# Performance work log

Hardware: AMD Instinct MI355X
Metric: run time of the kernel (lower is better)

Reference implementation:

```python
import jax, jax.numpy as jnp
import numpy as np

B, T, D, H, W = 512, 4096, 8, 16, 16  # batch, timesteps, data_size, hidden_size, width_size


def lipswish(x):
    return 0.909 * jax.nn.silu(x)


def _linear_params(key, out_f, in_f):
    kw, kb = jax.random.split(key)
    lim = 1.0 / np.sqrt(in_f)
    w = jax.random.uniform(kw, (out_f, in_f), minval=-lim, maxval=lim, dtype=jnp.float32)
    b = jax.random.uniform(kb, (out_f,), minval=-lim, maxval=lim, dtype=jnp.float32)
    return w, b


def setup_inputs() -> dict:
    key = jax.random.key(0)
    ks = jax.random.split(key, 9)
    ts = jnp.arange(T, dtype=jnp.float32)
    ys = jax.random.normal(ks[0], (B, T, D), dtype=jnp.float32)
    # initial MLP: (D+1) -> W -> H, relu hidden, identity final
    iW1, ib1 = _linear_params(ks[1], W, D + 1)
    iW2, ib2 = _linear_params(ks[2], H, W)
    # vf MLP: (H+1) -> W -> H, lipswish hidden, tanh final; scale=False -> ones (identity)
    vW1, vb1 = _linear_params(ks[3], W, H + 1)
    vW2, vb2 = _linear_params(ks[4], H, W)
    # cvf MLP: (H+1) -> W -> H*D, lipswish hidden, tanh final; scale=False -> ones
    cW1, cb1 = _linear_params(ks[5], W, H + 1)
    cW2, cb2 = _linear_params(ks[6], H * D, W)
    # readout: H -> 1
    rW, rb = _linear_params(ks[7], 1, H)
    return dict(ts=ts, ys=ys, iW1=iW1, ib1=ib1, iW2=iW2, ib2=ib2,
                vW1=vW1, vb1=vb1, vW2=vW2, vb2=vb2,
                cW1=cW1, cb1=cb1, cW2=cW2, cb2=cb2, rW=rW, rb=rb)


def reference(ts, ys, iW1, ib1, iW2, ib2, vW1, vb1, vW2, vb2,
              cW1, cb1, cW2, cb2, rW, rb):
    Bn, Tn, Dn = ys.shape
    Hn = iW2.shape[0]
    # initial hidden state: initial MLP on concat([t0, y0])
    init_in = jnp.concatenate([jnp.broadcast_to(ts[0], (Bn, 1)), ys[:, 0]], axis=1)  # (B, D+1)
    y0 = jax.nn.relu(init_in @ iW1.T + ib1) @ iW2.T + ib2  # (B, H)
    # Euler with dt=1 on integer-spaced ts: control increment = ys[n+1]-ys[n]
    dX = jnp.swapaxes(ys[:, 1:] - ys[:, :-1], 0, 1)  # (T-1, B, D)
    t_steps = ts[0] + jnp.arange(Tn - 1, dtype=ys.dtype)  # (T-1,)

    def step(y, inp):
        t, dx = inp  # scalar, (B, D)
        z = jnp.concatenate([jnp.broadcast_to(t, (Bn, 1)), y], axis=1)  # (B, H+1)
        f = jnp.tanh(lipswish(z @ vW1.T + vb1) @ vW2.T + vb2)           # (B, H) drift
        g = jnp.tanh(lipswish(z @ cW1.T + cb1) @ cW2.T + cb2)           # (B, H*D)
        g = g.reshape(Bn, Hn, Dn)
        y = y + f + jnp.einsum('bhd,bd->bh', g, dx)  # dt = 1.0
        return y, None

    yT, _ = jax.lax.scan(step, y0, (t_steps, dX))
    saved = jnp.stack([y0, yT], axis=1)  # SaveAt(t0=True, t1=True) -> (B, 2, H)
    return saved @ rW.T + rb  # (B, 2, 1)
```

## Files before the change

### kernel.cpp

```cpp
#include <hip/hip_runtime.h>

#define T_LEN 4096

typedef float v2f __attribute__((ext_vector_type(2)));
typedef float v4f __attribute__((ext_vector_type(4)));

__device__ __forceinline__ float frcp(float x) { return __builtin_amdgcn_rcpf(x); }
__device__ __forceinline__ float fexp2(float x) { return __builtin_amdgcn_exp2f(x); }

__device__ __forceinline__ void pk_fma_v(v2f& acc, v2f w, v2f s) {
  asm("v_pk_fma_f32 %0, %1, %2, %0" : "+v"(acc) : "v"(w), "v"(s));
}

template <int CTRL>
__device__ __forceinline__ float dpp_add(float x) {
  int t = __builtin_amdgcn_mov_dpp(__float_as_int(x), CTRL, 0xF, 0xF, true);
  return x + __int_as_float(t);
}

__device__ __forceinline__ void cfence() { asm volatile("" ::: "memory"); }

#define NLN2f (-0.6931471805599453f)

__device__ __forceinline__ float readout_lds(const float* cb,
                                             const float* __restrict__ rW,
                                             float rb0) {
  v4f a = *(const v4f*)(cb + 64);
  v4f b = *(const v4f*)(cb + 68);
  v4f c = *(const v4f*)(cb + 72);
  v4f d = *(const v4f*)(cb + 76);
  float o = rb0;
  o = fmaf(rW[0],  a.x, o); o = fmaf(rW[1],  a.y, o);
  o = fmaf(rW[2],  a.z, o); o = fmaf(rW[3],  a.w, o);
  o = fmaf(rW[4],  b.x, o); o = fmaf(rW[5],  b.y, o);
  o = fmaf(rW[6],  b.z, o); o = fmaf(rW[7],  b.w, o);
  o = fmaf(rW[8],  c.x, o); o = fmaf(rW[9],  c.y, o);
  o = fmaf(rW[10], c.z, o); o = fmaf(rW[11], c.w, o);
  o = fmaf(rW[12], d.x, o); o = fmaf(rW[13], d.y, o);
  o = fmaf(rW[14], d.z, o); o = fmaf(rW[15], d.w, o);
  return o;
}

__global__ __launch_bounds__(64) void disc_kernel(
    const float* __restrict__ ts, const float* __restrict__ ys,
    const float* __restrict__ iW1, const float* __restrict__ ib1,
    const float* __restrict__ iW2, const float* __restrict__ ib2,
    const float* __restrict__ vW1, const float* __restrict__ vb1,
    const float* __restrict__ vW2, const float* __restrict__ vb2,
    const float* __restrict__ cW1, const float* __restrict__ cb1,
    const float* __restrict__ cW2, const float* __restrict__ cb2,
    const float* __restrict__ rW, const float* __restrict__ rb,
    float* __restrict__ out)
{
  const int b   = blockIdx.x;
  const int l   = threadIdx.x;
  const int h16 = l & 15;
  const int p   = (l >> 4) & 1;
  const int hf  = l >> 2;
  const int d0  = (2 * l) & 7;
  const int q4  = 4 * (l & 3);
  const int ywslot = ((l & 3) == 0) ? (64 + hf) : (80 + l);

  __shared__ __align__(16) float sbuf[16];
  __shared__ __align__(16) float cbuf[160];
  __shared__ __align__(16) float xbuf[1024];

  const float* __restrict__ ysb = ys + (size_t)b * (T_LEN * 8);

  const float NL2E = -1.4426950408889634f;
  const float TSW  = 2.0f * 1.4426950408889634f * 0.909f;
  const float TSB  = 2.0f * 1.4426950408889634f;

  float w1t, b1m;
  v2f W1y2[8];
  {
    const float* W1 = p ? cW1 : vW1;
    const float* bv = p ? cb1 : vb1;
    w1t = NL2E * W1[h16 * 17];
    b1m = NL2E * bv[h16];
#pragma unroll
    for (int k = 0; k < 8; ++k) {
      v2f w; w.x = NL2E * W1[h16 * 17 + 1 + 2 * k];
             w.y = NL2E * W1[h16 * 17 + 2 + 2 * k];
      W1y2[k] = w;
    }
  }
  v2f W2q[2];
#pragma unroll
  for (int j = 0; j < 2; ++j) {
    v2f w; w.x = TSW * vW2[hf * 16 + q4 + 2 * j];
           w.y = TSW * vW2[hf * 16 + q4 + 2 * j + 1];
    W2q[j] = w;
  }
  v2f G0p[8], G1p[8];
#pragma unroll
  for (int k = 0; k < 8; ++k) {
    v2f c0; c0.x = TSW * cW2[(2 * l) * 16 + 2 * k]; c0.y = TSW * cW2[(2 * l) * 16 + 2 * k + 1];
    G0p[k] = c0;
    v2f c1; c1.x = TSW * cW2[(2 * l + 1) * 16 + 2 * k]; c1.y = TSW * cW2[(2 * l + 1) * 16 + 2 * k + 1];
    G1p[k] = c1;
  }
  const float b2p  = TSB * vb2[hf];
  const float bg0p = TSB * cb2[2 * l];
  const float bg1p = TSB * cb2[2 * l + 1];

  const float t0 = ts[0];

  float y_own;
  {
    float acc = ib1[h16] + iW1[h16 * 9] * t0;
#pragma unroll
    for (int d = 0; d < 8; ++d) acc = fmaf(iW1[h16 * 9 + 1 + d], ysb[d], acc);
    sbuf[h16] = fmaxf(acc, 0.0f);
    cfence();
    float acc2 = ib2[h16];
#pragma unroll
    for (int k = 0; k < 16; ++k) acc2 = fmaf(iW2[h16 * 16 + k], sbuf[k], acc2);
    cbuf[64 + h16] = acc2;
    cfence();
    y_own = cbuf[64 + hf];
  }

  {
    const float o = readout_lds(cbuf, rW, rb[0]);
    if (l == 0) out[2 * b] = o;
  }

  const int CLAMP = T_LEN * 8 - 4;
  float4 A, Bq, Cq, Dq;
  {
    const int f0 = l * 8;
    A  = *(const float4*)(ysb + min(f0,      CLAMP));
    Bq = *(const float4*)(ysb + min(f0 + 4,  CLAMP));
    Cq = *(const float4*)(ysb + min(f0 + 8,  CLAMP));
    Dq = *(const float4*)(ysb + min(f0 + 12, CLAMP));
    float4 e0, e1;
    e0.x = Cq.x - A.x;  e0.y = Cq.y - A.y;  e0.z = Cq.z - A.z;  e0.w = Cq.w - A.w;
    e1.x = Dq.x - Bq.x; e1.y = Dq.y - Bq.y; e1.z = Dq.z - Bq.z; e1.w = Dq.w - Bq.w;
    *(float4*)(xbuf + l * 8)     = e0;
    *(float4*)(xbuf + l * 8 + 4) = e1;
    cfence();
  }

  float t = t0;
  for (int c = 0; c < 64; ++c) {
    {
      const int cn = min(c + 1, 63);
      const int f0 = cn * 512 + l * 8;
      A  = *(const float4*)(ysb + min(f0,      CLAMP));
      Bq = *(const float4*)(ysb + min(f0 + 4,  CLAMP));
      Cq = *(const float4*)(ysb + min(f0 + 8,  CLAMP));
      Dq = *(const float4*)(ysb + min(f0 + 12, CLAMP));
    }
    const float* __restrict__ xb = xbuf + (c & 1) * 512;
    const int base = c * 64;
    const int nsteps = min(64, (T_LEN - 1) - base);
    for (int j = 0; j < nsteps; ++j) {
      const v4f ya = *(const v4f*)(cbuf + 64);
      const v4f yb = *(const v4f*)(cbuf + 68);
      const v4f yc = *(const v4f*)(cbuf + 72);
      const v4f yd = *(const v4f*)(cbuf + 76);
      const v2f dx = *(const v2f*)(xb + j * 8 + d0);

      const float m_t = fmaf(w1t, t, b1m);
      v2f ma; ma.x = m_t;  ma.y = 0.0f;
      v2f mb; mb.x = 0.0f; mb.y = 0.0f;
      pk_fma_v(ma, W1y2[0], ya.xy);
      pk_fma_v(ma, W1y2[1], ya.zw);
      pk_fma_v(ma, W1y2[2], yb.xy);
      pk_fma_v(ma, W1y2[3], yb.zw);
      pk_fma_v(mb, W1y2[4], yc.xy);
      pk_fma_v(mb, W1y2[5], yc.zw);
      pk_fma_v(mb, W1y2[6], yd.xy);
      pk_fma_v(mb, W1y2[7], yd.zw);
      const v2f ms = ma + mb;
      const float m = ms.x + ms.y;

      const float eM = fexp2(m);
      const float s  = (m * NLN2f) * frcp(1.0f + eM);

      cbuf[l] = s;
      cfence();
      const v4f g0 = *(const v4f*)(cbuf + 16);
      const v4f g1 = *(const v4f*)(cbuf + 20);
      const v4f g2 = *(const v4f*)(cbuf + 24);
      const v4f g3 = *(const v4f*)(cbuf + 28);
      const v4f sf = *(const v4f*)(cbuf + q4);

      v2f ga; ga.x = bg0p; ga.y = 0.0f;
      v2f gc; gc.x = 0.0f; gc.y = 0.0f;
      v2f gb; gb.x = bg1p; gb.y = 0.0f;
      v2f gd; gd.x = 0.0f; gd.y = 0.0f;
      pk_fma_v(ga, G0p[0], g0.xy); pk_fma_v(ga, G0p[1], g0.zw);
      pk_fma_v(ga, G0p[2], g1.xy); pk_fma_v(ga, G0p[3], g1.zw);
      pk_fma_v(gc, G0p[4], g2.xy); pk_fma_v(gc, G0p[5], g2.zw);
      pk_fma_v(gc, G0p[6], g3.xy); pk_fma_v(gc, G0p[7], g3.zw);
      pk_fma_v(gb, G1p[0], g0.xy); pk_fma_v(gb, G1p[1], g0.zw);
      pk_fma_v(gb, G1p[2], g1.xy); pk_fma_v(gb, G1p[3], g1.zw);
      pk_fma_v(gd, G1p[4], g2.xy); pk_fma_v(gd, G1p[5], g2.zw);
      pk_fma_v(gd, G1p[6], g3.xy); pk_fma_v(gd, G1p[7], g3.zw);

      v2f fa; fa.x = 0.0f; fa.y = 0.0f;
      pk_fma_v(fa, W2q[0], sf.xy);
      pk_fma_v(fa, W2q[1], sf.zw);
      float fp = fa.x + fa.y;
      fp = dpp_add<0xB1>(fp);
      fp = dpp_add<0x4E>(fp);
      const float farg = fp + b2p;

      const v2f gs0 = ga + gc;
      const v2f gs1 = gb + gd;
      const float g0v = fmaf(-2.0f, frcp(1.0f + fexp2(gs0.x + gs0.y)), 1.0f);
      const float g1v = fmaf(-2.0f, frcp(1.0f + fexp2(gs1.x + gs1.y)), 1.0f);
      const float fv  = fmaf(-2.0f, frcp(1.0f + fexp2(farg)), 1.0f);

      float pr = fmaf(g0v, dx.x, g1v * dx.y);
      pr = dpp_add<0xB1>(pr);
      pr = dpp_add<0x4E>(pr);

      y_own = y_own + (fv + pr);
      cbuf[ywslot] = y_own;
      cfence();
      t += 1.0f;
    }
    float* xbn = xbuf + ((c + 1) & 1) * 512;
    float4 e0, e1;
    e0.x = Cq.x - A.x;  e0.y = Cq.y - A.y;  e0.z = Cq.z - A.z;  e0.w = Cq.w - A.w;
    e1.x = Dq.x - Bq.x; e1.y = Dq.y - Bq.y; e1.z = Dq.z - Bq.z; e1.w = Dq.w - Bq.w;
    *(float4*)(xbn + l * 8)     = e0;
    *(float4*)(xbn + l * 8 + 4) = e1;
    cfence();
  }

  {
    const float o = readout_lds(cbuf, rW, rb[0]);
    if (l == 0) out[2 * b + 1] = o;
  }
}

extern "C" void kernel_launch(void* const* d_in, const int* in_sizes, int n_in,
                              void* d_out, int out_size, void* d_ws, size_t ws_size,
                              hipStream_t stream) {
  (void)in_sizes; (void)n_in; (void)out_size; (void)d_ws; (void)ws_size;
  const float* ts  = (const float*)d_in[0];
  const float* ys  = (const float*)d_in[1];
  const float* iW1 = (const float*)d_in[2];
  const float* ib1 = (const float*)d_in[3];
  const float* iW2 = (const float*)d_in[4];
  const float* ib2 = (const float*)d_in[5];
  const float* vW1 = (const float*)d_in[6];
  const float* vb1 = (const float*)d_in[7];
  const float* vW2 = (const float*)d_in[8];
  const float* vb2 = (const float*)d_in[9];
  const float* cW1 = (const float*)d_in[10];
  const float* cb1 = (const float*)d_in[11];
  const float* cW2 = (const float*)d_in[12];
  const float* cb2 = (const float*)d_in[13];
  const float* rW  = (const float*)d_in[14];
  const float* rb  = (const float*)d_in[15];
  float* out = (float*)d_out;
  hipLaunchKernelGGL(disc_kernel, dim3(512), dim3(64), 0, stream,
                     ts, ys, iW1, ib1, iW2, ib2, vW1, vb1, vW2, vb2,
                     cW1, cb1, cW2, cb2, rW, rb, out);
}
```

Before: 1.195 ms.

## Process two batch items per wavefront with interleaved independent recurrences

Each 64-lane block now advances two batch elements at once, with separate LDS state and control-increment buffers, and the instruction streams of the two recurrences are interleaved. The grid is halved to 256 blocks. The aim is to hide the latency of the serial per-step chain (LDS round trips, DPP reductions, exp/rcp) by giving the scheduler independent work within one wave. The cost is twice the instructions issued per wave and half as many waves, which on a device with many SIMDs may leave more of them idle.

```diff
diff --git a/kernel.cpp b/kernel.cpp
--- a/kernel.cpp
+++ b/kernel.cpp
@@ -52,7 +52,7 @@
     const float* __restrict__ rW, const float* __restrict__ rb,
     float* __restrict__ out)
 {
-  const int b   = blockIdx.x;
+  const int b0  = blockIdx.x * 2;
   const int l   = threadIdx.x;
   const int h16 = l & 15;
   const int p   = (l >> 4) & 1;
@@ -61,11 +61,15 @@
   const int q4  = 4 * (l & 3);
   const int ywslot = ((l & 3) == 0) ? (64 + hf) : (80 + l);
 
-  __shared__ __align__(16) float sbuf[16];
-  __shared__ __align__(16) float cbuf[160];
-  __shared__ __align__(16) float xbuf[1024];
-
-  const float* __restrict__ ysb = ys + (size_t)b * (T_LEN * 8);
+  __shared__ __align__(16) float sbuf0[16];
+  __shared__ __align__(16) float sbuf1[16];
+  __shared__ __align__(16) float cbuf0[160];
+  __shared__ __align__(16) float cbuf1[160];
+  __shared__ __align__(16) float xbuf0[1024];
+  __shared__ __align__(16) float xbuf1[1024];
+
+  const float* __restrict__ ysb0 = ys + (size_t)b0 * (T_LEN * 8);
+  const float* __restrict__ ysb1 = ysb0 + (size_t)(T_LEN * 8);
 
   const float NL2E = -1.4426950408889634f;
   const float TSW  = 2.0f * 1.4426950408889634f * 0.909f;
@@ -106,39 +110,65 @@
 
   const float t0 = ts[0];
 
-  float y_own;
-  {
-    float acc = ib1[h16] + iW1[h16 * 9] * t0;
-#pragma unroll
-    for (int d = 0; d < 8; ++d) acc = fmaf(iW1[h16 * 9 + 1 + d], ysb[d], acc);
-    sbuf[h16] = fmaxf(acc, 0.0f);
+  float y_own0, y_own1;
+  {
+    float a0 = ib1[h16] + iW1[h16 * 9] * t0;
+    float a1 = a0;
+#pragma unroll
+    for (int d = 0; d < 8; ++d) {
+      const float w = iW1[h16 * 9 + 1 + d];
+      a0 = fmaf(w, ysb0[d], a0);
+      a1 = fmaf(w, ysb1[d], a1);
+    }
+    sbuf0[h16] = fmaxf(a0, 0.0f);
+    sbuf1[h16] = fmaxf(a1, 0.0f);
     cfence();
-    float acc2 = ib2[h16];
-#pragma unroll
-    for (int k = 0; k < 16; ++k) acc2 = fmaf(iW2[h16 * 16 + k], sbuf[k], acc2);
-    cbuf[64 + h16] = acc2;
+    float c0 = ib2[h16];
+    float c1 = ib2[h16];
+#pragma unroll
+    for (int k = 0; k < 16; ++k) {
+      const float w = iW2[h16 * 16 + k];
+      c0 = fmaf(w, sbuf0[k], c0);
+      c1 = fmaf(w, sbuf1[k], c1);
+    }
+    cbuf0[64 + h16] = c0;
+    cbuf1[64 + h16] = c1;
     cfence();
-    y_own = cbuf[64 + hf];
-  }
-
-  {
-    const float o = readout_lds(cbuf, rW, rb[0]);
-    if (l == 0) out[2 * b] = o;
+    y_own0 = cbuf0[64 + hf];
+    y_own1 = cbuf1[64 + hf];
+  }
+
+  {
+    const float rb0 = rb[0];
+    const float o0 = readout_lds(cbuf0, rW, rb0);
+    const float o1 = readout_lds(cbuf1, rW, rb0);
+    if (l == 0) {
+      out[2 * b0]     = o0;
+      out[2 * b0 + 2] = o1;
+    }
   }
 
   const int CLAMP = T_LEN * 8 - 4;
-  float4 A, Bq, Cq, Dq;
+  float4 A0, B0, C0, D0, A1, B1, C1, D1;
   {
     const int f0 = l * 8;
-    A  = *(const float4*)(ysb + min(f0,      CLAMP));
-    Bq = *(const float4*)(ysb + min(f0 + 4,  CLAMP));
-    Cq = *(const float4*)(ysb + min(f0 + 8,  CLAMP));
-    Dq = *(const float4*)(ysb + min(f0 + 12, CLAMP));
+    A0 = *(const float4*)(ysb0 + min(f0,      CLAMP));
+    B0 = *(const float4*)(ysb0 + min(f0 + 4,  CLAMP));
+    C0 = *(const float4*)(ysb0 + min(f0 + 8,  CLAMP));
+    D0 = *(const float4*)(ysb0 + min(f0 + 12, CLAMP));
+    A1 = *(const float4*)(ysb1 + min(f0,      CLAMP));
+    B1 = *(const float4*)(ysb1 + min(f0 + 4,  CLAMP));
+    C1 = *(const float4*)(ysb1 + min(f0 + 8,  CLAMP));
+    D1 = *(const float4*)(ysb1 + min(f0 + 12, CLAMP));
     float4 e0, e1;
-    e0.x = Cq.x - A.x;  e0.y = Cq.y - A.y;  e0.z = Cq.z - A.z;  e0.w = Cq.w - A.w;
-    e1.x = Dq.x - Bq.x; e1.y = Dq.y - Bq.y; e1.z = Dq.z - Bq.z; e1.w = Dq.w - Bq.w;
-    *(float4*)(xbuf + l * 8)     = e0;
-    *(float4*)(xbuf + l * 8 + 4) = e1;
+    e0.x = C0.x - A0.x; e0.y = C0.y - A0.y; e0.z = C0.z - A0.z; e0.w = C0.w - A0.w;
+    e1.x = D0.x - B0.x; e1.y = D0.y - B0.y; e1.z = D0.z - B0.z; e1.w = D0.w - B0.w;
+    *(float4*)(xbuf0 + l * 8)     = e0;
+    *(float4*)(xbuf0 + l * 8 + 4) = e1;
+    e0.x = C1.x - A1.x; e0.y = C1.y - A1.y; e0.z = C1.z - A1.z; e0.w = C1.w - A1.w;
+    e1.x = D1.x - B1.x; e1.y = D1.y - B1.y; e1.z = D1.z - B1.z; e1.w = D1.w - B1.w;
+    *(float4*)(xbuf1 + l * 8)     = e0;
+    *(float4*)(xbuf1 + l * 8 + 4) = e1;
     cfence();
   }
 
@@ -147,94 +177,149 @@
     {
       const int cn = min(c + 1, 63);
       const int f0 = cn * 512 + l * 8;
-      A  = *(const float4*)(ysb + min(f0,      CLAMP));
-      Bq = *(const float4*)(ysb + min(f0 + 4,  CLAMP));
-      Cq = *(const float4*)(ysb + min(f0 + 8,  CLAMP));
-      Dq = *(const float4*)(ysb + min(f0 + 12, CLAMP));
-    }
-    const float* __restrict__ xb = xbuf + (c & 1) * 512;
+      A0 = *(const float4*)(ysb0 + min(f0,      CLAMP));
+      B0 = *(const float4*)(ysb0 + min(f0 + 4,  CLAMP));
+      C0 = *(const float4*)(ysb0 + min(f0 + 8,  CLAMP));
+      D0 = *(const float4*)(ysb0 + min(f0 + 12, CLAMP));
+      A1 = *(const float4*)(ysb1 + min(f0,      CLAMP));
+      B1 = *(const float4*)(ysb1 + min(f0 + 4,  CLAMP));
+      C1 = *(const float4*)(ysb1 + min(f0 + 8,  CLAMP));
+      D1 = *(const float4*)(ysb1 + min(f0 + 12, CLAMP));
+    }
+    const float* __restrict__ xb0 = xbuf0 + (c & 1) * 512;
+    const float* __restrict__ xb1 = xbuf1 + (c & 1) * 512;
     const int base = c * 64;
     const int nsteps = min(64, (T_LEN - 1) - base);
     for (int j = 0; j < nsteps; ++j) {
-      const v4f ya = *(const v4f*)(cbuf + 64);
-      const v4f yb = *(const v4f*)(cbuf + 68);
-      const v4f yc = *(const v4f*)(cbuf + 72);
-      const v4f yd = *(const v4f*)(cbuf + 76);
-      const v2f dx = *(const v2f*)(xb + j * 8 + d0);
+      const v4f ya0 = *(const v4f*)(cbuf0 + 64);
+      const v4f yb0 = *(const v4f*)(cbuf0 + 68);
+      const v4f yc0 = *(const v4f*)(cbuf0 + 72);
+      const v4f yd0 = *(const v4f*)(cbuf0 + 76);
+      const v4f ya1 = *(const v4f*)(cbuf1 + 64);
+      const v4f yb1 = *(const v4f*)(cbuf1 + 68);
+      const v4f yc1 = *(const v4f*)(cbuf1 + 72);
+      const v4f yd1 = *(const v4f*)(cbuf1 + 76);
+      const v2f dx0 = *(const v2f*)(xb0 + j * 8 + d0);
+      const v2f dx1 = *(const v2f*)(xb1 + j * 8 + d0);
 
       const float m_t = fmaf(w1t, t, b1m);
-      v2f ma; ma.x = m_t;  ma.y = 0.0f;
-      v2f mb; mb.x = 0.0f; mb.y = 0.0f;
-      pk_fma_v(ma, W1y2[0], ya.xy);
-      pk_fma_v(ma, W1y2[1], ya.zw);
-      pk_fma_v(ma, W1y2[2], yb.xy);
-      pk_fma_v(ma, W1y2[3], yb.zw);
-      pk_fma_v(mb, W1y2[4], yc.xy);
-      pk_fma_v(mb, W1y2[5], yc.zw);
-      pk_fma_v(mb, W1y2[6], yd.xy);
-      pk_fma_v(mb, W1y2[7], yd.zw);
-      const v2f ms = ma + mb;
-      const float m = ms.x + ms.y;
-
-      const float eM = fexp2(m);
-      const float s  = (m * NLN2f) * frcp(1.0f + eM);
-
-      cbuf[l] = s;
+      v2f ma0; ma0.x = m_t;  ma0.y = 0.0f;
+      v2f mb0; mb0.x = 0.0f; mb0.y = 0.0f;
+      v2f ma1; ma1.x = m_t;  ma1.y = 0.0f;
+      v2f mb1; mb1.x = 0.0f; mb1.y = 0.0f;
+      pk_fma_v(ma0, W1y2[0], ya0.xy); pk_fma_v(ma1, W1y2[0], ya1.xy);
+      pk_fma_v(ma0, W1y2[1], ya0.zw); pk_fma_v(ma1, W1y2[1], ya1.zw);
+      pk_fma_v(ma0, W1y2[2], yb0.xy); pk_fma_v(ma1, W1y2[2], yb1.xy);
+      pk_fma_v(ma0, W1y2[3], yb0.zw); pk_fma_v(ma1, W1y2[3], yb1.zw);
+      pk_fma_v(mb0, W1y2[4], yc0.xy); pk_fma_v(mb1, W1y2[4], yc1.xy);
+      pk_fma_v(mb0, W1y2[5], yc0.zw); pk_fma_v(mb1, W1y2[5], yc1.zw);
+      pk_fma_v(mb0, W1y2[6], yd0.xy); pk_fma_v(mb1, W1y2[6], yd1.xy);
+      pk_fma_v(mb0, W1y2[7], yd0.zw); pk_fma_v(mb1, W1y2[7], yd1.zw);
+      const v2f ms0 = ma0 + mb0;
+      const v2f ms1 = ma1 + mb1;
+      const float m0 = ms0.x + ms0.y;
+      const float m1 = ms1.x + ms1.y;
+
+      const float eM0 = fexp2(m0);
+      const float eM1 = fexp2(m1);
+      const float s0 = (m0 * NLN2f) * frcp(1.0f + eM0);
+      const float s1 = (m1 * NLN2f) * frcp(1.0f + eM1);
+
+      cbuf0[l] = s0;
+      cbuf1[l] = s1;
       cfence();
-      const v4f g0 = *(const v4f*)(cbuf + 16);
-      const v4f g1 = *(const v4f*)(cbuf + 20);
-      const v4f g2 = *(const v4f*)(cbuf + 24);
-      const v4f g3 = *(const v4f*)(cbuf + 28);
-      const v4f sf = *(const v4f*)(cbuf + q4);
-
-      v2f ga; ga.x = bg0p; ga.y = 0.0f;
-      v2f gc; gc.x = 0.0f; gc.y = 0.0f;
-      v2f gb; gb.x = bg1p; gb.y = 0.0f;
-      v2f gd; gd.x = 0.0f; gd.y = 0.0f;
-      pk_fma_v(ga, G0p[0], g0.xy); pk_fma_v(ga, G0p[1], g0.zw);
-      pk_fma_v(ga, G0p[2], g1.xy); pk_fma_v(ga, G0p[3], g1.zw);
-      pk_fma_v(gc, G0p[4], g2.xy); pk_fma_v(gc, G0p[5], g2.zw);
-      pk_fma_v(gc, G0p[6], g3.xy); pk_fma_v(gc, G0p[7], g3.zw);
-      pk_fma_v(gb, G1p[0], g0.xy); pk_fma_v(gb, G1p[1], g0.zw);
-      pk_fma_v(gb, G1p[2], g1.xy); pk_fma_v(gb, G1p[3], g1.zw);
-      pk_fma_v(gd, G1p[4], g2.xy); pk_fma_v(gd, G1p[5], g2.zw);
-      pk_fma_v(gd, G1p[6], g3.xy); pk_fma_v(gd, G1p[7], g3.zw);
-
-      v2f fa; fa.x = 0.0f; fa.y = 0.0f;
-      pk_fma_v(fa, W2q[0], sf.xy);
-      pk_fma_v(fa, W2q[1], sf.zw);
-      float fp = fa.x + fa.y;
-      fp = dpp_add<0xB1>(fp);
-      fp = dpp_add<0x4E>(fp);
-      const float farg = fp + b2p;
-
-      const v2f gs0 = ga + gc;
-      const v2f gs1 = gb + gd;
-      const float g0v = fmaf(-2.0f, frcp(1.0f + fexp2(gs0.x + gs0.y)), 1.0f);
-      const float g1v = fmaf(-2.0f, frcp(1.0f + fexp2(gs1.x + gs1.y)), 1.0f);
-      const float fv  = fmaf(-2.0f, frcp(1.0f + fexp2(farg)), 1.0f);
-
-      float pr = fmaf(g0v, dx.x, g1v * dx.y);
-      pr = dpp_add<0xB1>(pr);
-      pr = dpp_add<0x4E>(pr);
-
-      y_own = y_own + (fv + pr);
-      cbuf[ywslot] = y_own;
+      const v4f g00 = *(const v4f*)(cbuf0 + 16);
+      const v4f g10 = *(const v4f*)(cbuf0 + 20);
+      const v4f g20 = *(const v4f*)(cbuf0 + 24);
+      const v4f g30 = *(const v4f*)(cbuf0 + 28);
+      const v4f sf0 = *(const v4f*)(cbuf0 + q4);
+      const v4f g01 = *(const v4f*)(cbuf1 + 16);
+      const v4f g11 = *(const v4f*)(cbuf1 + 20);
+      const v4f g21 = *(const v4f*)(cbuf1 + 24);
+      const v4f g31 = *(const v4f*)(cbuf1 + 28);
+      const v4f sf1 = *(const v4f*)(cbuf1 + q4);
+
+      v2f ga0; ga0.x = bg0p; ga0.y = 0.0f;
+      v2f gc0; gc0.x = 0.0f; gc0.y = 0.0f;
+      v2f gb0; gb0.x = bg1p; gb0.y = 0.0f;
+      v2f gd0; gd0.x = 0.0f; gd0.y = 0.0f;
+      v2f ga1; ga1.x = bg0p; ga1.y = 0.0f;
+      v2f gc1; gc1.x = 0.0f; gc1.y = 0.0f;
+      v2f gb1; gb1.x = bg1p; gb1.y = 0.0f;
+      v2f gd1; gd1.x = 0.0f; gd1.y = 0.0f;
+      pk_fma_v(ga0, G0p[0], g00.xy); pk_fma_v(ga1, G0p[0], g01.xy);
+      pk_fma_v(ga0, G0p[1], g00.zw); pk_fma_v(ga1, G0p[1], g01.zw);
+      pk_fma_v(ga0, G0p[2], g10.xy); pk_fma_v(ga1, G0p[2], g11.xy);
+      pk_fma_v(ga0, G0p[3], g10.zw); pk_fma_v(ga1, G0p[3], g11.zw);
+      pk_fma_v(gc0, G0p[4], g20.xy); pk_fma_v(gc1, G0p[4], g21.xy);
+      pk_fma_v(gc0, G0p[5], g20.zw); pk_fma_v(gc1, G0p[5], g21.zw);
+      pk_fma_v(gc0, G0p[6], g30.xy); pk_fma_v(gc1, G0p[6], g31.xy);
+      pk_fma_v(gc0, G0p[7], g30.zw); pk_fma_v(gc1, G0p[7], g31.zw);
+      pk_fma_v(gb0, G1p[0], g00.xy); pk_fma_v(gb1, G1p[0], g01.xy);
+      pk_fma_v(gb0, G1p[1], g00.zw); pk_fma_v(gb1, G1p[1], g01.zw);
+      pk_fma_v(gb0, G1p[2], g10.xy); pk_fma_v(gb1, G1p[2], g11.xy);
+      pk_fma_v(gb0, G1p[3], g10.zw); pk_fma_v(gb1, G1p[3], g11.zw);
+      pk_fma_v(gd0, G1p[4], g20.xy); pk_fma_v(gd1, G1p[4], g21.xy);
+      pk_fma_v(gd0, G1p[5], g20.zw); pk_fma_v(gd1, G1p[5], g21.zw);
+      pk_fma_v(gd0, G1p[6], g30.xy); pk_fma_v(gd1, G1p[6], g31.xy);
+      pk_fma_v(gd0, G1p[7], g30.zw); pk_fma_v(gd1, G1p[7], g31.zw);
+
+      v2f fa0; fa0.x = 0.0f; fa0.y = 0.0f;
+      v2f fa1; fa1.x = 0.0f; fa1.y = 0.0f;
+      pk_fma_v(fa0, W2q[0], sf0.xy); pk_fma_v(fa1, W2q[0], sf1.xy);
+      pk_fma_v(fa0, W2q[1], sf0.zw); pk_fma_v(fa1, W2q[1], sf1.zw);
+      float fp0 = fa0.x + fa0.y;
+      float fp1 = fa1.x + fa1.y;
+      fp0 = dpp_add<0xB1>(fp0); fp1 = dpp_add<0xB1>(fp1);
+      fp0 = dpp_add<0x4E>(fp0); fp1 = dpp_add<0x4E>(fp1);
+      const float farg0 = fp0 + b2p;
+      const float farg1 = fp1 + b2p;
+
+      const v2f gs00 = ga0 + gc0;
+      const v2f gs10 = gb0 + gd0;
+      const v2f gs01 = ga1 + gc1;
+      const v2f gs11 = gb1 + gd1;
+      const float g0v0 = fmaf(-2.0f, frcp(1.0f + fexp2(gs00.x + gs00.y)), 1.0f);
+      const float g1v0 = fmaf(-2.0f, frcp(1.0f + fexp2(gs10.x + gs10.y)), 1.0f);
+      const float g0v1 = fmaf(-2.0f, frcp(1.0f + fexp2(gs01.x + gs01.y)), 1.0f);
+      const float g1v1 = fmaf(-2.0f, frcp(1.0f + fexp2(gs11.x + gs11.y)), 1.0f);
+      const float fv0 = fmaf(-2.0f, frcp(1.0f + fexp2(farg0)), 1.0f);
+      const float fv1 = fmaf(-2.0f, frcp(1.0f + fexp2(farg1)), 1.0f);
+
+      float pr0 = fmaf(g0v0, dx0.x, g1v0 * dx0.y);
+      float pr1 = fmaf(g0v1, dx1.x, g1v1 * dx1.y);
+      pr0 = dpp_add<0xB1>(pr0); pr1 = dpp_add<0xB1>(pr1);
+      pr0 = dpp_add<0x4E>(pr0); pr1 = dpp_add<0x4E>(pr1);
+
+      y_own0 = y_own0 + (fv0 + pr0);
+      y_own1 = y_own1 + (fv1 + pr1);
+      cbuf0[ywslot] = y_own0;
+      cbuf1[ywslot] = y_own1;
       cfence();
       t += 1.0f;
     }
-    float* xbn = xbuf + ((c + 1) & 1) * 512;
+    float* xbn0 = xbuf0 + ((c + 1) & 1) * 512;
+    float* xbn1 = xbuf1 + ((c + 1) & 1) * 512;
     float4 e0, e1;
-    e0.x = Cq.x - A.x;  e0.y = Cq.y - A.y;  e0.z = Cq.z - A.z;  e0.w = Cq.w - A.w;
-    e1.x = Dq.x - Bq.x; e1.y = Dq.y - Bq.y; e1.z = Dq.z - Bq.z; e1.w = Dq.w - Bq.w;
-    *(float4*)(xbn + l * 8)     = e0;
-    *(float4*)(xbn + l * 8 + 4) = e1;
+    e0.x = C0.x - A0.x; e0.y = C0.y - A0.y; e0.z = C0.z - A0.z; e0.w = C0.w - A0.w;
+    e1.x = D0.x - B0.x; e1.y = D0.y - B0.y; e1.z = D0.z - B0.z; e1.w = D0.w - B0.w;
+    *(float4*)(xbn0 + l * 8)     = e0;
+    *(float4*)(xbn0 + l * 8 + 4) = e1;
+    e0.x = C1.x - A1.x; e0.y = C1.y - A1.y; e0.z = C1.z - A1.z; e0.w = C1.w - A1.w;
+    e1.x = D1.x - B1.x; e1.y = D1.y - B1.y; e1.z = D1.z - B1.z; e1.w = D1.w - B1.w;
+    *(float4*)(xbn1 + l * 8)     = e0;
+    *(float4*)(xbn1 + l * 8 + 4) = e1;
     cfence();
   }
 
   {
-    const float o = readout_lds(cbuf, rW, rb[0]);
-    if (l == 0) out[2 * b + 1] = o;
+    const float rb0 = rb[0];
+    const float o0 = readout_lds(cbuf0, rW, rb0);
+    const float o1 = readout_lds(cbuf1, rW, rb0);
+    if (l == 0) {
+      out[2 * b0 + 1] = o0;
+      out[2 * b0 + 3] = o1;
+    }
   }
 }
 
@@ -259,7 +344,7 @@
   const float* rW  = (const float*)d_in[14];
   const float* rb  = (const float*)d_in[15];
   float* out = (float*)d_out;
-  hipLaunchKernelGGL(disc_kernel, dim3(512), dim3(64), 0, stream,
+  hipLaunchKernelGGL(disc_kernel, dim3(256), dim3(64), 0, stream,
                      ts, ys, iW1, ib1, iW2, ib2, vW1, vb1, vW2, vb2,
                      cW1, cb1, cW2, cb2, rW, rb, out);
 }
```

New measurement: 1.939 ms. 1.62x slower.

## Split per-step MLP across lane quads with ds_bpermute and DPP reductions

Applied to the files above, without the earlier changes.

Reorganises the per-timestep work so each lane quad holds a slice of both hidden layers' weights, computing partial dot products that are reduced with DPP instead of each lane doing full 16-wide dot products. The hidden state and activations now travel between lanes through ds_bpermute rather than LDS stores and broadcast loads, and the per-step LDS write of y is moved to after the loop. The aim is to cut the serial per-step latency on the recurrence's critical path. In exchange each step issues 12 bpermutes plus extra DPP moves and selects.

```diff
diff --git a/kernel.cpp b/kernel.cpp
--- a/kernel.cpp
+++ b/kernel.cpp
@@ -16,6 +16,19 @@
 __device__ __forceinline__ float dpp_add(float x) {
   int t = __builtin_amdgcn_mov_dpp(__float_as_int(x), CTRL, 0xF, 0xF, true);
   return x + __int_as_float(t);
+}
+template <int CTRL>
+__device__ __forceinline__ float dpp_movf(float x) {
+  return __int_as_float(
+      __builtin_amdgcn_mov_dpp(__float_as_int(x), CTRL, 0xF, 0xF, true));
+}
+template <int CTRL>
+__device__ __forceinline__ v2f dpp_mov2(v2f x) {
+  v2f r; r.x = dpp_movf<CTRL>(x.x); r.y = dpp_movf<CTRL>(x.y); return r;
+}
+
+__device__ __forceinline__ float bperm(int idx, float v) {
+  return __int_as_float(__builtin_amdgcn_ds_bpermute(idx, __float_as_int(v)));
 }
 
 __device__ __forceinline__ void cfence() { asm volatile("" ::: "memory"); }
@@ -55,11 +68,11 @@
   const int b   = blockIdx.x;
   const int l   = threadIdx.x;
   const int h16 = l & 15;
-  const int p   = (l >> 4) & 1;
-  const int hf  = l >> 2;
-  const int d0  = (2 * l) & 7;
-  const int q4  = 4 * (l & 3);
-  const int ywslot = ((l & 3) == 0) ? (64 + hf) : (80 + l);
+  const int a   = (l >> 4) & 3;
+  const int c   = l & 3;
+  const int q   = l >> 2;
+  const int d0  = 2 * c;
+  const int ywslot = (c == 0) ? (64 + q) : (80 + l);
 
   __shared__ __align__(16) float sbuf[16];
   __shared__ __align__(16) float cbuf[160];
@@ -71,36 +84,36 @@
   const float TSW  = 2.0f * 1.4426950408889634f * 0.909f;
   const float TSB  = 2.0f * 1.4426950408889634f;
 
-  float w1t, b1m;
-  v2f W1y2[8];
-  {
-    const float* W1 = p ? cW1 : vW1;
-    const float* bv = p ? cb1 : vb1;
-    w1t = NL2E * W1[h16 * 17];
-    b1m = NL2E * bv[h16];
-#pragma unroll
-    for (int k = 0; k < 8; ++k) {
-      v2f w; w.x = NL2E * W1[h16 * 17 + 1 + 2 * k];
-             w.y = NL2E * W1[h16 * 17 + 2 + 2 * k];
-      W1y2[k] = w;
+  int idx0 = 4 * (16 * c + 0  + a);
+  int idx1 = 4 * (16 * c + 4  + a);
+  int idx2 = 4 * (16 * c + 8  + a);
+  int idx3 = 4 * (16 * c + 12 + a);
+
+  float W1v4[4], W1c4[4];
+#pragma unroll
+  for (int j = 0; j < 4; ++j) {
+    W1v4[j] = NL2E * vW1[q * 17 + 1 + 4 * c + j];
+    W1c4[j] = NL2E * cW1[q * 17 + 1 + 4 * c + j];
+  }
+  const float w1t0 = (c == 0) ? NL2E * vW1[q * 17] : 0.0f;
+  const float b1m0 = (c == 0) ? NL2E * vb1[q]      : 0.0f;
+  const float w1t1 = (c == 0) ? NL2E * cW1[q * 17] : 0.0f;
+  const float b1m1 = (c == 0) ? NL2E * cb1[q]      : 0.0f;
+  float W2f4[4];
+#pragma unroll
+  for (int j = 0; j < 4; ++j) W2f4[j] = TSW * vW2[q * 16 + 4 * c + j];
+  v2f Gp[4][4];
+#pragma unroll
+  for (int e = 0; e < 4; ++e) {
+#pragma unroll
+    for (int j = 0; j < 4; ++j) {
+      v2f w;
+      w.x = TSW * cW2[(8 * q + 2 * e)     * 16 + 4 * c + j];
+      w.y = TSW * cW2[(8 * q + 2 * e + 1) * 16 + 4 * c + j];
+      Gp[e][j] = w;
     }
   }
-  v2f W2q[2];
-#pragma unroll
-  for (int j = 0; j < 2; ++j) {
-    v2f w; w.x = TSW * vW2[hf * 16 + q4 + 2 * j];
-           w.y = TSW * vW2[hf * 16 + q4 + 2 * j + 1];
-    W2q[j] = w;
-  }
-  v2f G0p[8], G1p[8];
-#pragma unroll
-  for (int k = 0; k < 8; ++k) {
-    v2f c0; c0.x = TSW * cW2[(2 * l) * 16 + 2 * k]; c0.y = TSW * cW2[(2 * l) * 16 + 2 * k + 1];
-    G0p[k] = c0;
-    v2f c1; c1.x = TSW * cW2[(2 * l + 1) * 16 + 2 * k]; c1.y = TSW * cW2[(2 * l + 1) * 16 + 2 * k + 1];
-    G1p[k] = c1;
-  }
-  const float b2p  = TSB * vb2[hf];
+  const float b2p  = TSB * vb2[q];
   const float bg0p = TSB * cb2[2 * l];
   const float bg1p = TSB * cb2[2 * l + 1];
 
@@ -118,7 +131,7 @@
     for (int k = 0; k < 16; ++k) acc2 = fmaf(iW2[h16 * 16 + k], sbuf[k], acc2);
     cbuf[64 + h16] = acc2;
     cfence();
-    y_own = cbuf[64 + hf];
+    y_own = cbuf[64 + q];
   }
 
   {
@@ -143,75 +156,91 @@
   }
 
   float t = t0;
-  for (int c = 0; c < 64; ++c) {
+  for (int ch = 0; ch < 64; ++ch) {
     {
-      const int cn = min(c + 1, 63);
+      const int cn = min(ch + 1, 63);
       const int f0 = cn * 512 + l * 8;
       A  = *(const float4*)(ysb + min(f0,      CLAMP));
       Bq = *(const float4*)(ysb + min(f0 + 4,  CLAMP));
       Cq = *(const float4*)(ysb + min(f0 + 8,  CLAMP));
       Dq = *(const float4*)(ysb + min(f0 + 12, CLAMP));
     }
-    const float* __restrict__ xb = xbuf + (c & 1) * 512;
-    const int base = c * 64;
+    const float* __restrict__ xb = xbuf + (ch & 1) * 512;
+    const int base = ch * 64;
     const int nsteps = min(64, (T_LEN - 1) - base);
     for (int j = 0; j < nsteps; ++j) {
-      const v4f ya = *(const v4f*)(cbuf + 64);
-      const v4f yb = *(const v4f*)(cbuf + 68);
-      const v4f yc = *(const v4f*)(cbuf + 72);
-      const v4f yd = *(const v4f*)(cbuf + 76);
       const v2f dx = *(const v2f*)(xb + j * 8 + d0);
 
-      const float m_t = fmaf(w1t, t, b1m);
-      v2f ma; ma.x = m_t;  ma.y = 0.0f;
-      v2f mb; mb.x = 0.0f; mb.y = 0.0f;
-      pk_fma_v(ma, W1y2[0], ya.xy);
-      pk_fma_v(ma, W1y2[1], ya.zw);
-      pk_fma_v(ma, W1y2[2], yb.xy);
-      pk_fma_v(ma, W1y2[3], yb.zw);
-      pk_fma_v(mb, W1y2[4], yc.xy);
-      pk_fma_v(mb, W1y2[5], yc.zw);
-      pk_fma_v(mb, W1y2[6], yd.xy);
-      pk_fma_v(mb, W1y2[7], yd.zw);
-      const v2f ms = ma + mb;
-      const float m = ms.x + ms.y;
-
-      const float eM = fexp2(m);
-      const float s  = (m * NLN2f) * frcp(1.0f + eM);
-
-      cbuf[l] = s;
-      cfence();
-      const v4f g0 = *(const v4f*)(cbuf + 16);
-      const v4f g1 = *(const v4f*)(cbuf + 20);
-      const v4f g2 = *(const v4f*)(cbuf + 24);
-      const v4f g3 = *(const v4f*)(cbuf + 28);
-      const v4f sf = *(const v4f*)(cbuf + q4);
-
-      v2f ga; ga.x = bg0p; ga.y = 0.0f;
-      v2f gc; gc.x = 0.0f; gc.y = 0.0f;
-      v2f gb; gb.x = bg1p; gb.y = 0.0f;
-      v2f gd; gd.x = 0.0f; gd.y = 0.0f;
-      pk_fma_v(ga, G0p[0], g0.xy); pk_fma_v(ga, G0p[1], g0.zw);
-      pk_fma_v(ga, G0p[2], g1.xy); pk_fma_v(ga, G0p[3], g1.zw);
-      pk_fma_v(gc, G0p[4], g2.xy); pk_fma_v(gc, G0p[5], g2.zw);
-      pk_fma_v(gc, G0p[6], g3.xy); pk_fma_v(gc, G0p[7], g3.zw);
-      pk_fma_v(gb, G1p[0], g0.xy); pk_fma_v(gb, G1p[1], g0.zw);
-      pk_fma_v(gb, G1p[2], g1.xy); pk_fma_v(gb, G1p[3], g1.zw);
-      pk_fma_v(gd, G1p[4], g2.xy); pk_fma_v(gd, G1p[5], g2.zw);
-      pk_fma_v(gd, G1p[6], g3.xy); pk_fma_v(gd, G1p[7], g3.zw);
-
-      v2f fa; fa.x = 0.0f; fa.y = 0.0f;
-      pk_fma_v(fa, W2q[0], sf.xy);
-      pk_fma_v(fa, W2q[1], sf.zw);
-      float fp = fa.x + fa.y;
-      fp = dpp_add<0xB1>(fp);
-      fp = dpp_add<0x4E>(fp);
+      const float yg0 = bperm(idx0, y_own);
+      const float yg1 = bperm(idx1, y_own);
+      const float yg2 = bperm(idx2, y_own);
+      const float yg3 = bperm(idx3, y_own);
+
+      float acc0 = fmaf(w1t0, t, b1m0);
+      float acc1 = fmaf(w1t1, t, b1m1);
+      acc0 = fmaf(W1v4[0], yg0, acc0);
+      acc0 = fmaf(W1v4[1], yg1, acc0);
+      acc0 = fmaf(W1v4[2], yg2, acc0);
+      acc0 = fmaf(W1v4[3], yg3, acc0);
+      acc1 = fmaf(W1c4[0], yg0, acc1);
+      acc1 = fmaf(W1c4[1], yg1, acc1);
+      acc1 = fmaf(W1c4[2], yg2, acc1);
+      acc1 = fmaf(W1c4[3], yg3, acc1);
+      acc0 = dpp_add<0xB1>(acc0); acc0 = dpp_add<0x4E>(acc0);
+      acc1 = dpp_add<0xB1>(acc1); acc1 = dpp_add<0x4E>(acc1);
+
+      const float eM0 = fexp2(acc0);
+      const float s0v = (acc0 * NLN2f) * frcp(1.0f + eM0);
+      const float eM1 = fexp2(acc1);
+      const float s1v = (acc1 * NLN2f) * frcp(1.0f + eM1);
+
+      const float sg00 = bperm(idx0, s0v);
+      const float sg01 = bperm(idx1, s0v);
+      const float sg02 = bperm(idx2, s0v);
+      const float sg03 = bperm(idx3, s0v);
+      const float sg10 = bperm(idx0, s1v);
+      const float sg11 = bperm(idx1, s1v);
+      const float sg12 = bperm(idx2, s1v);
+      const float sg13 = bperm(idx3, s1v);
+
+      v2f sd0; sd0.x = sg10; sd0.y = sg10;
+      v2f sd1; sd1.x = sg11; sd1.y = sg11;
+      v2f sd2; sd2.x = sg12; sd2.y = sg12;
+      v2f sd3; sd3.x = sg13; sd3.y = sg13;
+      v2f P0; P0.x = 0.0f; P0.y = 0.0f;
+      v2f P1; P1.x = 0.0f; P1.y = 0.0f;
+      v2f P2; P2.x = 0.0f; P2.y = 0.0f;
+      v2f P3; P3.x = 0.0f; P3.y = 0.0f;
+      pk_fma_v(P0, Gp[0][0], sd0); pk_fma_v(P0, Gp[0][1], sd1);
+      pk_fma_v(P0, Gp[0][2], sd2); pk_fma_v(P0, Gp[0][3], sd3);
+      pk_fma_v(P1, Gp[1][0], sd0); pk_fma_v(P1, Gp[1][1], sd1);
+      pk_fma_v(P1, Gp[1][2], sd2); pk_fma_v(P1, Gp[1][3], sd3);
+      pk_fma_v(P2, Gp[2][0], sd0); pk_fma_v(P2, Gp[2][1], sd1);
+      pk_fma_v(P2, Gp[2][2], sd2); pk_fma_v(P2, Gp[2][3], sd3);
+      pk_fma_v(P3, Gp[3][0], sd0); pk_fma_v(P3, Gp[3][1], sd1);
+      pk_fma_v(P3, Gp[3][2], sd2); pk_fma_v(P3, Gp[3][3], sd3);
+
+      float fp = W2f4[0] * sg00;
+      fp = fmaf(W2f4[1], sg01, fp);
+      fp = fmaf(W2f4[2], sg02, fp);
+      fp = fmaf(W2f4[3], sg03, fp);
+      fp = dpp_add<0xB1>(fp); fp = dpp_add<0x4E>(fp);
       const float farg = fp + b2p;
 
-      const v2f gs0 = ga + gc;
-      const v2f gs1 = gb + gd;
-      const float g0v = fmaf(-2.0f, frcp(1.0f + fexp2(gs0.x + gs0.y)), 1.0f);
-      const float g1v = fmaf(-2.0f, frcp(1.0f + fexp2(gs1.x + gs1.y)), 1.0f);
+      const bool s2b = (c & 2) != 0;
+      const bool s1b = (c & 1) != 0;
+      v2f K0 = s2b ? P2 : P0;  v2f X0 = s2b ? P0 : P2;
+      v2f K1 = s2b ? P3 : P1;  v2f X1 = s2b ? P1 : P3;
+      v2f R0 = dpp_mov2<0x4E>(X0);
+      v2f R1 = dpp_mov2<0x4E>(X1);
+      v2f Q0 = K0 + R0;
+      v2f Q1 = K1 + R1;
+      v2f K = s1b ? Q1 : Q0;  v2f X = s1b ? Q0 : Q1;
+      v2f R = dpp_mov2<0xB1>(X);
+      const v2f G = K + R;
+
+      const float g0v = fmaf(-2.0f, frcp(1.0f + fexp2(G.x + bg0p)), 1.0f);
+      const float g1v = fmaf(-2.0f, frcp(1.0f + fexp2(G.y + bg1p)), 1.0f);
       const float fv  = fmaf(-2.0f, frcp(1.0f + fexp2(farg)), 1.0f);
 
       float pr = fmaf(g0v, dx.x, g1v * dx.y);
@@ -219,11 +248,9 @@
       pr = dpp_add<0x4E>(pr);
 
       y_own = y_own + (fv + pr);
-      cbuf[ywslot] = y_own;
-      cfence();
       t += 1.0f;
     }
-    float* xbn = xbuf + ((c + 1) & 1) * 512;
+    float* xbn = xbuf + ((ch + 1) & 1) * 512;
     float4 e0, e1;
     e0.x = Cq.x - A.x;  e0.y = Cq.y - A.y;  e0.z = Cq.z - A.z;  e0.w = Cq.w - A.w;
     e1.x = Dq.x - Bq.x; e1.y = Dq.y - Bq.y; e1.z = Dq.z - Bq.z; e1.w = Dq.w - Bq.w;
@@ -232,6 +259,8 @@
     cfence();
   }
 
+  cbuf[ywslot] = y_own;
+  cfence();
   {
     const float o = readout_lds(cbuf, rW, rb[0]);
     if (l == 0) out[2 * b + 1] = o;
```

Measured after the change: 1.288 ms. 1.08x slower.

## Split first-layer dot product across wave halves and prefetch next-step state

Applied to the files above, without the earlier changes.

Each lane now computes only half of the 16-term hidden-state dot product for the first MLP layer, using lanes 0-31 and 32-63 for the two halves. The partial sums are combined with a v_permlane32_swap cross-half exchange. The y-state and dx loads for the next step are issued at the end of the current iteration, so LDS latency overlaps the loop back-edge instead of sitting at the top. This trades four packed FMAs per step for a cross-lane swap instruction and reorders loads on the serial recurrence's critical path. xbuf is padded so the one-past-end dx prefetch stays in bounds.

```diff
diff --git a/kernel.cpp b/kernel.cpp
--- a/kernel.cpp
+++ b/kernel.cpp
@@ -16,6 +16,14 @@
 __device__ __forceinline__ float dpp_add(float x) {
   int t = __builtin_amdgcn_mov_dpp(__float_as_int(x), CTRL, 0xF, 0xF, true);
   return x + __int_as_float(t);
+}
+
+__device__ __forceinline__ float half_sum(float x) {
+  float a = x, b;
+  asm("v_mov_b32 %1, %0\n\t"
+      "v_permlane32_swap_b32 %0, %1"
+      : "+v"(a), "=&v"(b));
+  return a + b;
 }
 
 __device__ __forceinline__ void cfence() { asm volatile("" ::: "memory"); }
@@ -52,18 +60,19 @@
     const float* __restrict__ rW, const float* __restrict__ rb,
     float* __restrict__ out)
 {
-  const int b   = blockIdx.x;
-  const int l   = threadIdx.x;
-  const int h16 = l & 15;
-  const int p   = (l >> 4) & 1;
-  const int hf  = l >> 2;
-  const int d0  = (2 * l) & 7;
-  const int q4  = 4 * (l & 3);
+  const int b    = blockIdx.x;
+  const int l    = threadIdx.x;
+  const int h16  = l & 15;
+  const int p    = (l >> 4) & 1;
+  const int hf   = l >> 2;
+  const int d0   = (2 * l) & 7;
+  const int q4   = 4 * (l & 3);
+  const int hoff = (l >> 5) * 8;
   const int ywslot = ((l & 3) == 0) ? (64 + hf) : (80 + l);
 
   __shared__ __align__(16) float sbuf[16];
   __shared__ __align__(16) float cbuf[160];
-  __shared__ __align__(16) float xbuf[1024];
+  __shared__ __align__(16) float xbuf[1040];
 
   const float* __restrict__ ysb = ys + (size_t)b * (T_LEN * 8);
 
@@ -72,18 +81,20 @@
   const float TSB  = 2.0f * 1.4426950408889634f;
 
   float w1t, b1m;
-  v2f W1y2[8];
+  v2f W1y2[4];
   {
     const float* W1 = p ? cW1 : vW1;
     const float* bv = p ? cb1 : vb1;
     w1t = NL2E * W1[h16 * 17];
     b1m = NL2E * bv[h16];
-#pragma unroll
-    for (int k = 0; k < 8; ++k) {
-      v2f w; w.x = NL2E * W1[h16 * 17 + 1 + 2 * k];
-             w.y = NL2E * W1[h16 * 17 + 2 + 2 * k];
+    const int cbase = 1 + hoff;
+#pragma unroll
+    for (int k = 0; k < 4; ++k) {
+      v2f w; w.x = NL2E * W1[h16 * 17 + cbase + 2 * k];
+             w.y = NL2E * W1[h16 * 17 + cbase + 2 * k + 1];
       W1y2[k] = w;
     }
+    if (l >= 32) { w1t = 0.0f; b1m = 0.0f; }
   }
   v2f W2q[2];
 #pragma unroll
@@ -141,6 +152,10 @@
     *(float4*)(xbuf + l * 8 + 4) = e1;
     cfence();
   }
+
+  v4f ya = *(const v4f*)(cbuf + 64 + hoff);
+  v4f yb = *(const v4f*)(cbuf + 64 + hoff + 4);
+  v2f dxc = *(const v2f*)(xbuf + d0);
 
   float t = t0;
   for (int c = 0; c < 64; ++c) {
@@ -156,25 +171,15 @@
     const int base = c * 64;
     const int nsteps = min(64, (T_LEN - 1) - base);
     for (int j = 0; j < nsteps; ++j) {
-      const v4f ya = *(const v4f*)(cbuf + 64);
-      const v4f yb = *(const v4f*)(cbuf + 68);
-      const v4f yc = *(const v4f*)(cbuf + 72);
-      const v4f yd = *(const v4f*)(cbuf + 76);
-      const v2f dx = *(const v2f*)(xb + j * 8 + d0);
+      const v2f dx = dxc;
 
       const float m_t = fmaf(w1t, t, b1m);
-      v2f ma; ma.x = m_t;  ma.y = 0.0f;
-      v2f mb; mb.x = 0.0f; mb.y = 0.0f;
-      pk_fma_v(ma, W1y2[0], ya.xy);
-      pk_fma_v(ma, W1y2[1], ya.zw);
-      pk_fma_v(ma, W1y2[2], yb.xy);
-      pk_fma_v(ma, W1y2[3], yb.zw);
-      pk_fma_v(mb, W1y2[4], yc.xy);
-      pk_fma_v(mb, W1y2[5], yc.zw);
-      pk_fma_v(mb, W1y2[6], yd.xy);
-      pk_fma_v(mb, W1y2[7], yd.zw);
-      const v2f ms = ma + mb;
-      const float m = ms.x + ms.y;
+      v2f acc; acc.x = m_t; acc.y = 0.0f;
+      pk_fma_v(acc, W1y2[0], ya.xy);
+      pk_fma_v(acc, W1y2[1], ya.zw);
+      pk_fma_v(acc, W1y2[2], yb.xy);
+      pk_fma_v(acc, W1y2[3], yb.zw);
+      const float m = half_sum(acc.x + acc.y);
 
       const float eM = fexp2(m);
       const float s  = (m * NLN2f) * frcp(1.0f + eM);
@@ -221,6 +226,9 @@
       y_own = y_own + (fv + pr);
       cbuf[ywslot] = y_own;
       cfence();
+      ya = *(const v4f*)(cbuf + 64 + hoff);
+      yb = *(const v4f*)(cbuf + 64 + hoff + 4);
+      dxc = *(const v2f*)(xb + (j + 1) * 8 + d0);
       t += 1.0f;
     }
     float* xbn = xbuf + ((c + 1) & 1) * 512;
@@ -230,6 +238,7 @@
     *(float4*)(xbn + l * 8)     = e0;
     *(float4*)(xbn + l * 8 + 4) = e1;
     cfence();
+    dxc = *(const v2f*)(xbn + d0);
   }
 
   {
```

Result: faster. 1.113 ms (-6.9%).
